# Kernel optimization log

Hardware: AMD Instinct MI355X
Metric: run time of the kernel (lower is better)

Reference implementation:

```python
import jax, jax.numpy as jnp
import numpy as np

# dims: L=seq_len, N=batch, C=embed_dim, H=heads, D=head_dim, W=window_size
L, N, C, H, D, W = 1024, 4, 2048, 16, 128, 512
ROPE_BASE = 10000.0
SCALE = 1.0 / np.sqrt(D).astype(np.float32)


def _rope(x, cos, sin):
    # interleaved-pair rotary embedding; x: (..., D), cos/sin broadcast to (..., D//2)
    x1, x2 = x[..., 0::2], x[..., 1::2]
    return jnp.stack([x1 * cos - x2 * sin, x1 * sin + x2 * cos], axis=-1).reshape(x.shape)


def setup_inputs() -> dict:
    key = jax.random.key(0)
    ks = jax.random.split(key, 4)
    s = 0.02
    return {
        "x": jax.random.normal(ks[0], (L, N, C), jnp.float32),
        "wq": jax.random.normal(ks[1], (C, C), jnp.float32) * s,
        "bq": jnp.zeros((C,), jnp.float32),
        "wkv": jax.random.normal(ks[2], (2 * C, C), jnp.float32) * s,
        "bkv": jnp.zeros((2 * C,), jnp.float32),
        "wo": jax.random.normal(ks[3], (C, C), jnp.float32) * s,
        "bo": jnp.zeros((C,), jnp.float32),
        "alibi_slopes": jnp.asarray(2.0 ** (-8.0 * np.arange(1, H + 1) / H), jnp.float32),
    }


def reference(x, wq, bq, wkv, bkv, wo, bo, alibi_slopes):
    # x: (L, N, C) -> batch-major (N, L, C)
    xb = jnp.transpose(x, (1, 0, 2))
    q = (xb @ wq.T + bq).reshape(N, L, H, D)
    # memory=None path: zero input cache, cache_mask all False
    cache = jnp.zeros((N, W, C), x.dtype)
    kv_cache = cache @ wkv.T + bkv          # detached in original; masked out anyway
    kv_cur = xb @ wkv.T + bkv
    kv = jnp.concatenate([kv_cache, kv_cur], axis=1).reshape(N, L + W, 2, H, D)
    # RoPE over absolute kv positions [0, L+W); queries live at positions [W, W+L)
    t = jnp.arange(L + W, dtype=jnp.float32)
    inv_freq = 1.0 / (ROPE_BASE ** (jnp.arange(0, D, 2, dtype=jnp.float32) / D))
    freqs = jnp.outer(t, inv_freq)          # (L+W, D//2)
    cos, sin = jnp.cos(freqs), jnp.sin(freqs)
    q = _rope(q, cos[W:W + L][None, :, None, :], sin[W:W + L][None, :, None, :])
    k = _rope(kv[:, :, 0], cos[None, :, None, :], sin[None, :, None, :])
    v = kv[:, :, 1]
    scores = jnp.einsum('bihd,bjhd->bhij', q, k) * SCALE  # (N,H,L,L+W)
    i = jnp.arange(L)[:, None]
    j = jnp.arange(L + W)[None, :]
    # causal sliding window: query at kv-position i+W attends j in [i, i+W];
    # kv_mask is False for the (empty) cache region j < W
    mask = (j >= i) & (j <= i + W) & (j >= W)
    bias = alibi_slopes[:, None, None] * (j - i - W).astype(jnp.float32)  # <= 0 in window
    scores = jnp.where(mask[None, None], scores + bias[None], -jnp.inf)
    p = jax.nn.softmax(scores, axis=-1)
    attn = jnp.einsum('bhij,bjhd->bihd', p, v).reshape(N, L, C)
    out = attn @ wo.T + bo
    return jnp.transpose(out, (1, 0, 2))    # (L, N, C)
```

## Files before the change

kernel.cpp:

```cpp
#include <hip/hip_runtime.h>
#include <hip/hip_bf16.h>

typedef __attribute__((ext_vector_type(4))) float f32x4;
typedef __attribute__((ext_vector_type(8))) short s16x8;
typedef __attribute__((ext_vector_type(4))) short s16x4;
typedef __attribute__((ext_vector_type(4))) int i32x4;

__device__ __forceinline__ short f2bf(float f) {
    union { __hip_bfloat16 h; short s; } u;
    u.h = __float2bfloat16(f);
    return u.s;
}

#define GLD16(g, l) __builtin_amdgcn_global_load_lds((const __attribute__((address_space(1))) void*)(g), (__attribute__((address_space(3))) void*)(l), 16, 0, 0)
#define MFMA16(a, b, c) __builtin_amdgcn_mfma_f32_16x16x32_bf16((a), (b), (c), 0, 0, 0)

__global__ void conv_lin(const float* __restrict__ in, short* __restrict__ out, int n4) {
    int i = blockIdx.x * blockDim.x + threadIdx.x;
    int stride = gridDim.x * blockDim.x;
    for (; i < n4; i += stride) {
        float4 v = reinterpret_cast<const float4*>(in)[i];
        s16x4 o;
        o[0] = f2bf(v.x); o[1] = f2bf(v.y); o[2] = f2bf(v.z); o[3] = f2bf(v.w);
        reinterpret_cast<s16x4*>(out)[i] = o;
    }
}

__global__ void conv_x(const float* __restrict__ x, short* __restrict__ Xb) {
    const int total = 1024 * 4 * 2048 / 4;
    int i = blockIdx.x * blockDim.x + threadIdx.x;
    int stride = gridDim.x * blockDim.x;
    for (; i < total; i += stride) {
        float4 v = reinterpret_cast<const float4*>(x)[i];
        int c4 = i & 511;
        int n  = (i >> 9) & 3;
        int l  = i >> 11;
        s16x4 o;
        o[0] = f2bf(v.x); o[1] = f2bf(v.y); o[2] = f2bf(v.z); o[3] = f2bf(v.w);
        reinterpret_cast<s16x4*>(Xb)[(n * 1024 + l) * 512 + c4] = o;
    }
}

__global__ void rope_tab(float* __restrict__ ctab, float* __restrict__ stab) {
    int l = blockIdx.x, t = threadIdx.x;
    float pos = (float)(512 + l);
    float inv = __expf(-9.210340371976184f * ((float)t * (1.0f / 64.0f)));
    float a = pos * inv;
    float s, c;
    sincosf(a, &s, &c);
    ctab[l * 64 + t] = c;
    stab[l * 64 + t] = s;
}

__device__ __forceinline__ void gemm128(const short* __restrict__ A, const short* __restrict__ B,
                                        short* As, short* Bs, f32x4 acc[4][4], int m0, int j0) {
    const int K = 2048;
    const int tid = threadIdx.x;
    const int lane = tid & 63;
    const int w = tid >> 6;
    const int wr = w >> 1, wc = w & 1;
    const int r8 = lane >> 3;
    const int cc = ((lane & 7) ^ r8) << 3;
    const size_t rowA0 = (size_t)(m0 + w * 32 + r8);
    const size_t rowB0 = (size_t)(j0 + w * 32 + r8);
    for (int kt = 0; kt < K; kt += 64) {
        #pragma unroll
        for (int q = 0; q < 4; ++q) {
            GLD16(A + (rowA0 + q * 8) * K + kt + cc, As + (w * 32 + q * 8) * 64);
            GLD16(B + (rowB0 + q * 8) * K + kt + cc, Bs + (w * 32 + q * 8) * 64);
        }
        __syncthreads();
        #pragma unroll
        for (int kk = 0; kk < 2; ++kk) {
            s16x8 af[4], bfv[4];
            #pragma unroll
            for (int mi = 0; mi < 4; ++mi) {
                int row = wr * 64 + mi * 16 + (lane & 15);
                int byte = row * 128 + ((kk * 64 + (lane >> 4) * 16) ^ ((row & 7) << 4));
                af[mi] = *reinterpret_cast<const s16x8*>(reinterpret_cast<const char*>(As) + byte);
            }
            #pragma unroll
            for (int nj = 0; nj < 4; ++nj) {
                int row = wc * 64 + nj * 16 + (lane & 15);
                int byte = row * 128 + ((kk * 64 + (lane >> 4) * 16) ^ ((row & 7) << 4));
                bfv[nj] = *reinterpret_cast<const s16x8*>(reinterpret_cast<const char*>(Bs) + byte);
            }
            #pragma unroll
            for (int mi = 0; mi < 4; ++mi)
                #pragma unroll
                for (int nj = 0; nj < 4; ++nj)
                    acc[mi][nj] = MFMA16(af[mi], bfv[nj], acc[mi][nj]);
        }
        __syncthreads();
    }
}

__global__ __launch_bounds__(256, 4)
void gemm_qkv(const short* __restrict__ Xb, const short* __restrict__ Wqkv,
              const float* __restrict__ bq, const float* __restrict__ bkv,
              const float* __restrict__ ctab, const float* __restrict__ stab,
              short* __restrict__ Qr, short* __restrict__ Kr, short* __restrict__ Vr) {
    __shared__ short As[8192], Bs[8192];
    const int m0 = blockIdx.y * 128, j0 = blockIdx.x * 128;
    f32x4 acc[4][4];
    #pragma unroll
    for (int a = 0; a < 4; ++a)
        #pragma unroll
        for (int b = 0; b < 4; ++b)
            #pragma unroll
            for (int r = 0; r < 4; ++r) acc[a][b][r] = 0.f;
    gemm128(Xb, Wqkv, As, Bs, acc, m0, j0);

    const int tid = threadIdx.x, lane = tid & 63, w = tid >> 6;
    const int wr = w >> 1, wc = w & 1;
    const int region = j0 >> 11;
    #pragma unroll
    for (int mi = 0; mi < 4; ++mi) {
        #pragma unroll
        for (int nj = 0; nj < 4; ++nj) {
            int col = j0 + wc * 64 + nj * 16 + (lane & 15);
            int h = (col >> 7) & 15;
            int d = col & 127;
            #pragma unroll
            for (int r = 0; r < 4; ++r) {
                int row = m0 + wr * 64 + mi * 16 + (lane >> 4) * 4 + r;
                int n = row >> 10, l = row & 1023;
                float v = acc[mi][nj][r];
                size_t oidx = (((size_t)(n * 16 + h)) * 1024 + l) * 128 + d;
                if (region == 0) {
                    v += bq[col];
                    float other = __shfl_xor(v, 1, 64);
                    float cs = ctab[l * 64 + (d >> 1)];
                    float sn = stab[l * 64 + (d >> 1)];
                    float o = (d & 1) ? (other * sn + v * cs) : (v * cs - other * sn);
                    Qr[oidx] = f2bf(o * 0.08838834764831843f);
                } else if (region == 1) {
                    v += bkv[col - 2048];
                    float other = __shfl_xor(v, 1, 64);
                    float cs = ctab[l * 64 + (d >> 1)];
                    float sn = stab[l * 64 + (d >> 1)];
                    float o = (d & 1) ? (other * sn + v * cs) : (v * cs - other * sn);
                    Kr[oidx] = f2bf(o);
                } else {
                    v += bkv[col - 2048];
                    Vr[oidx] = f2bf(v);
                }
            }
        }
    }
}

__global__ __launch_bounds__(256, 4)
void gemm_out(const short* __restrict__ Attn, const short* __restrict__ Wo,
              const float* __restrict__ bo, float* __restrict__ out) {
    __shared__ short As[8192], Bs[8192];
    const int m0 = blockIdx.y * 128, j0 = blockIdx.x * 128;
    f32x4 acc[4][4];
    #pragma unroll
    for (int a = 0; a < 4; ++a)
        #pragma unroll
        for (int b = 0; b < 4; ++b)
            #pragma unroll
            for (int r = 0; r < 4; ++r) acc[a][b][r] = 0.f;
    gemm128(Attn, Wo, As, Bs, acc, m0, j0);

    const int tid = threadIdx.x, lane = tid & 63, w = tid >> 6;
    const int wr = w >> 1, wc = w & 1;
    #pragma unroll
    for (int mi = 0; mi < 4; ++mi)
        #pragma unroll
        for (int nj = 0; nj < 4; ++nj) {
            int col = j0 + wc * 64 + nj * 16 + (lane & 15);
            #pragma unroll
            for (int r = 0; r < 4; ++r) {
                int row = m0 + wr * 64 + mi * 16 + (lane >> 4) * 4 + r;
                int n = row >> 10, l = row & 1023;
                out[((size_t)(l * 4 + n)) * 2048 + col] = acc[mi][nj][r] + bo[col];
            }
        }
}

__global__ __launch_bounds__(256, 2)
void attn_fwd(const short* __restrict__ Qr, const short* __restrict__ Kr,
              const short* __restrict__ Vr, const float* __restrict__ slopes,
              short* __restrict__ Attn) {
    __shared__ short Ks[64 * 128];
    __shared__ short Vts[128 * 64];
    __shared__ short Ps[4][2048];

    const int b = blockIdx.x;
    const int nh = (b & 7) * 8 + ((b >> 3) & 7);
    const int i0 = (b >> 6) * 128;
    const int n = nh >> 4, h = nh & 15;
    const short* Qh = Qr + (size_t)nh * (1024 * 128);
    const short* Kh = Kr + (size_t)nh * (1024 * 128);
    const short* Vh = Vr + (size_t)nh * (1024 * 128);
    const float slope = slopes[h];
    const int tid = threadIdx.x, lane = tid & 63, w = tid >> 6;

    s16x8 qf[2][4];
    #pragma unroll
    for (int mi = 0; mi < 2; ++mi)
        #pragma unroll
        for (int kk = 0; kk < 4; ++kk) {
            int row = i0 + w * 32 + mi * 16 + (lane & 15);
            qf[mi][kk] = *reinterpret_cast<const s16x8*>(Qh + (size_t)row * 128 + kk * 32 + (lane >> 4) * 8);
        }

    f32x4 oacc[2][8];
    #pragma unroll
    for (int mi = 0; mi < 2; ++mi)
        #pragma unroll
        for (int dj = 0; dj < 8; ++dj)
            #pragma unroll
            for (int r = 0; r < 4; ++r) oacc[mi][dj][r] = 0.f;
    float mrun[2][4], lrun[2][4];
    #pragma unroll
    for (int mi = 0; mi < 2; ++mi)
        #pragma unroll
        for (int r = 0; r < 4; ++r) { mrun[mi][r] = -1e30f; lrun[mi][r] = 0.f; }

    const int jlo = (i0 >= 512) ? (i0 - 512) : 0;
    const int jhi = i0 + 127;
    for (int j0 = jlo; j0 <= jhi; j0 += 64) {
        #pragma unroll
        for (int q = 0; q < 4; ++q) {
            int rbase = w * 16 + q * 4;
            int rloc = rbase + (lane >> 4);
            int lc = ((lane & 15) ^ (rloc & 7)) << 3;
            GLD16(Kh + (size_t)(j0 + rloc) * 128 + lc, Ks + rbase * 128);
        }
        #pragma unroll
        for (int p = 0; p < 4; ++p) {
            int d0 = (w + p * 4) * 8;
            int jj = j0 + lane;
            i32x4 vv = *reinterpret_cast<const i32x4*>(Vh + (size_t)jj * 128 + d0);
            const short* vs = reinterpret_cast<const short*>(&vv);
            #pragma unroll
            for (int e = 0; e < 8; ++e) {
                int d = d0 + e;
                int byte = d * 128 + ((lane * 2) ^ ((d & 7) << 4));
                *reinterpret_cast<short*>(reinterpret_cast<char*>(Vts) + byte) = vs[e];
            }
        }
        __syncthreads();

        f32x4 sacc[2][4];
        #pragma unroll
        for (int mi = 0; mi < 2; ++mi)
            #pragma unroll
            for (int nj = 0; nj < 4; ++nj)
                #pragma unroll
                for (int r = 0; r < 4; ++r) sacc[mi][nj][r] = 0.f;
        #pragma unroll
        for (int kk = 0; kk < 4; ++kk) {
            s16x8 kf[4];
            #pragma unroll
            for (int nj = 0; nj < 4; ++nj) {
                int kr = nj * 16 + (lane & 15);
                int byte = kr * 256 + ((kk * 64 + (lane >> 4) * 16) ^ ((kr & 7) << 4));
                kf[nj] = *reinterpret_cast<const s16x8*>(reinterpret_cast<const char*>(Ks) + byte);
            }
            #pragma unroll
            for (int mi = 0; mi < 2; ++mi)
                #pragma unroll
                for (int nj = 0; nj < 4; ++nj)
                    sacc[mi][nj] = MFMA16(qf[mi][kk], kf[nj], sacc[mi][nj]);
        }

        #pragma unroll
        for (int mi = 0; mi < 2; ++mi) {
            #pragma unroll
            for (int r = 0; r < 4; ++r) {
                int iq = i0 + w * 32 + mi * 16 + (lane >> 4) * 4 + r;
                float mx = -1e30f;
                #pragma unroll
                for (int nj = 0; nj < 4; ++nj) {
                    int jj = j0 + nj * 16 + (lane & 15);
                    float v = -1e30f;
                    if (jj <= iq && jj >= iq - 512)
                        v = sacc[mi][nj][r] + slope * (float)(jj - iq);
                    sacc[mi][nj][r] = v;
                    mx = fmaxf(mx, v);
                }
                #pragma unroll
                for (int s = 1; s < 16; s <<= 1) mx = fmaxf(mx, __shfl_xor(mx, s, 64));
                float mnew = fmaxf(mrun[mi][r], mx);
                float sf = __expf(mrun[mi][r] - mnew);
                mrun[mi][r] = mnew;
                lrun[mi][r] *= sf;
                #pragma unroll
                for (int dj = 0; dj < 8; ++dj) oacc[mi][dj][r] *= sf;
                float rs = 0.f;
                #pragma unroll
                for (int nj = 0; nj < 4; ++nj) {
                    float v = sacc[mi][nj][r];
                    float p = (v < -1e29f) ? 0.f : __expf(v - mnew);
                    sacc[mi][nj][r] = p;
                    rs += p;
                }
                #pragma unroll
                for (int s = 1; s < 16; s <<= 1) rs += __shfl_xor(rs, s, 64);
                lrun[mi][r] += rs;
            }
        }

        char* Pw = reinterpret_cast<char*>(&Ps[w][0]);
        #pragma unroll
        for (int mi = 0; mi < 2; ++mi)
            #pragma unroll
            for (int nj = 0; nj < 4; ++nj)
                #pragma unroll
                for (int r = 0; r < 4; ++r) {
                    int prow = mi * 16 + (lane >> 4) * 4 + r;
                    int cb = (nj * 16 + (lane & 15)) * 2;
                    int byte = prow * 128 + (cb ^ ((prow & 7) << 4));
                    *reinterpret_cast<short*>(Pw + byte) = f2bf(sacc[mi][nj][r]);
                }

        #pragma unroll
        for (int ks = 0; ks < 2; ++ks) {
            s16x8 pf[2];
            #pragma unroll
            for (int mi = 0; mi < 2; ++mi) {
                int prow = mi * 16 + (lane & 15);
                int byte = prow * 128 + (((ks * 32 + (lane >> 4) * 8) * 2) ^ ((prow & 7) << 4));
                pf[mi] = *reinterpret_cast<const s16x8*>(Pw + byte);
            }
            #pragma unroll
            for (int dj = 0; dj < 8; ++dj) {
                int d = dj * 16 + (lane & 15);
                int byte = d * 128 + (((ks * 32 + (lane >> 4) * 8) * 2) ^ ((d & 7) << 4));
                s16x8 vf = *reinterpret_cast<const s16x8*>(reinterpret_cast<const char*>(Vts) + byte);
                #pragma unroll
                for (int mi = 0; mi < 2; ++mi)
                    oacc[mi][dj] = MFMA16(pf[mi], vf, oacc[mi][dj]);
            }
        }
        __syncthreads();
    }

    #pragma unroll
    for (int mi = 0; mi < 2; ++mi)
        #pragma unroll
        for (int dj = 0; dj < 8; ++dj)
            #pragma unroll
            for (int r = 0; r < 4; ++r) {
                int iq = i0 + w * 32 + mi * 16 + (lane >> 4) * 4 + r;
                int d = dj * 16 + (lane & 15);
                float v = oacc[mi][dj][r] / lrun[mi][r];
                Attn[((size_t)(n * 1024 + iq)) * 2048 + h * 128 + d] = f2bf(v);
            }
}

extern "C" void kernel_launch(void* const* d_in, const int* in_sizes, int n_in,
                              void* d_out, int out_size, void* d_ws, size_t ws_size,
                              hipStream_t stream) {
    const float* x      = (const float*)d_in[0];
    const float* wq     = (const float*)d_in[1];
    const float* bq     = (const float*)d_in[2];
    const float* wkv    = (const float*)d_in[3];
    const float* bkv    = (const float*)d_in[4];
    const float* wo     = (const float*)d_in[5];
    const float* bo     = (const float*)d_in[6];
    const float* slopes = (const float*)d_in[7];
    float* out = (float*)d_out;

    char* ws = (char*)d_ws;
    size_t off = 0;
    auto alloc = [&](size_t bytes) { char* p = ws + off; off += (bytes + 255) & ~(size_t)255; return p; };
    float* ctab = (float*)alloc((size_t)1024 * 64 * 4);
    float* stab = (float*)alloc((size_t)1024 * 64 * 4);
    short* Xb   = (short*)alloc((size_t)4096 * 2048 * 2);
    short* Wqkv = (short*)alloc((size_t)6144 * 2048 * 2);
    short* Wo   = (short*)alloc((size_t)2048 * 2048 * 2);
    short* Qr   = (short*)alloc((size_t)64 * 1024 * 128 * 2);
    short* Kr   = (short*)alloc((size_t)64 * 1024 * 128 * 2);
    short* Vr   = (short*)alloc((size_t)64 * 1024 * 128 * 2);
    short* Attn = (short*)alloc((size_t)4096 * 2048 * 2);

    conv_x<<<2048, 256, 0, stream>>>(x, Xb);
    conv_lin<<<1024, 256, 0, stream>>>(wq, Wqkv, 2048 * 2048 / 4);
    conv_lin<<<2048, 256, 0, stream>>>(wkv, Wqkv + (size_t)2048 * 2048, 4096 * 2048 / 4);
    conv_lin<<<1024, 256, 0, stream>>>(wo, Wo, 2048 * 2048 / 4);
    rope_tab<<<1024, 64, 0, stream>>>(ctab, stab);
    gemm_qkv<<<dim3(48, 32), 256, 0, stream>>>(Xb, Wqkv, bq, bkv, ctab, stab, Qr, Kr, Vr);
    attn_fwd<<<512, 256, 0, stream>>>(Qr, Kr, Vr, slopes, Attn);
    gemm_out<<<dim3(16, 32), 256, 0, stream>>>(Attn, Wo, bo, out);
}
```

Baseline: 244.8 us.

## Pipeline QKV and output GEMMs with 8-wave 256x128 tiles and multi-stage LDS

Replaces the single-buffered 128x128 GEMM core with an 8-wave (512-thread) 256x128 tile that double-buffers K slices in LDS. Global-to-LDS loads for future slices are issued while MFMAs run, with manual waitcnt, barriers and setprio. Blocks are remapped to a 1D grid with an XCD-aware swizzle across column tiles. This aims to hide memory latency and improve L2 locality, but the epilogue still indexes only 4 waves' worth of rows (wr = w>>1 now spans 0..3 with 64-row stride, matching a 256-row tile), so correctness depends on that mapping holding.

```diff
diff --git a/kernel.cpp b/kernel.cpp
--- a/kernel.cpp
+++ b/kernel.cpp
@@ -52,64 +52,92 @@
     stab[l * 64 + t] = s;
 }
 
-__device__ __forceinline__ void gemm128(const short* __restrict__ A, const short* __restrict__ B,
-                                        short* As, short* Bs, f32x4 acc[4][4], int m0, int j0) {
-    const int K = 2048;
-    const int tid = threadIdx.x;
-    const int lane = tid & 63;
-    const int w = tid >> 6;
-    const int wr = w >> 1, wc = w & 1;
-    const int r8 = lane >> 3;
-    const int cc = ((lane & 7) ^ r8) << 3;
-    const size_t rowA0 = (size_t)(m0 + w * 32 + r8);
-    const size_t rowB0 = (size_t)(j0 + w * 32 + r8);
-    for (int kt = 0; kt < K; kt += 64) {
-        #pragma unroll
-        for (int q = 0; q < 4; ++q) {
-            GLD16(A + (rowA0 + q * 8) * K + kt + cc, As + (w * 32 + q * 8) * 64);
-            GLD16(B + (rowB0 + q * 8) * K + kt + cc, Bs + (w * 32 + q * 8) * 64);
-        }
-        __syncthreads();
-        #pragma unroll
-        for (int kk = 0; kk < 2; ++kk) {
-            s16x8 af[4], bfv[4];
-            #pragma unroll
-            for (int mi = 0; mi < 4; ++mi) {
-                int row = wr * 64 + mi * 16 + (lane & 15);
-                int byte = row * 128 + ((kk * 64 + (lane >> 4) * 16) ^ ((row & 7) << 4));
-                af[mi] = *reinterpret_cast<const s16x8*>(reinterpret_cast<const char*>(As) + byte);
-            }
-            #pragma unroll
-            for (int nj = 0; nj < 4; ++nj) {
-                int row = wc * 64 + nj * 16 + (lane & 15);
-                int byte = row * 128 + ((kk * 64 + (lane >> 4) * 16) ^ ((row & 7) << 4));
-                bfv[nj] = *reinterpret_cast<const s16x8*>(reinterpret_cast<const char*>(Bs) + byte);
-            }
-            #pragma unroll
-            for (int mi = 0; mi < 4; ++mi)
-                #pragma unroll
-                for (int nj = 0; nj < 4; ++nj)
-                    acc[mi][nj] = MFMA16(af[mi], bfv[nj], acc[mi][nj]);
-        }
-        __syncthreads();
-    }
-}
-
-__global__ __launch_bounds__(256, 4)
+
+__device__ __forceinline__ void stageA(const short* __restrict__ G, int rowbase, int kbase,
+                                       short* dst, int tid) {
+    #pragma unroll
+    for (int q = 0; q < 2; ++q) {
+        int chunk = q * 512 + tid;
+        GLD16(G + (size_t)(rowbase + (chunk >> 2)) * 2048 + kbase + ((chunk & 3) << 3),
+              dst + q * 4096 + (tid & ~63) * 8);
+    }
+}
+__device__ __forceinline__ void stageB(const short* __restrict__ G, int rowbase, int kbase,
+                                       short* dst, int tid) {
+    GLD16(G + (size_t)(rowbase + (tid >> 2)) * 2048 + kbase + ((tid & 3) << 3),
+          dst + (tid & ~63) * 8);
+}
+
+__device__ __forceinline__ void gemm_core8(const short* __restrict__ Aop, const short* __restrict__ Bop,
+                                           short* AL, short* BL, f32x4 acc[4][4], int m0, int j0) {
+    const int tid = threadIdx.x, lane = tid & 63;
+    const int w = tid >> 6, wr = w >> 1, wc = w & 1;
+
+    auto STG = [&](int sk, int skh) {
+        int kb = (sk & 31) * 64 + skh * 32;
+        stageA(Aop, m0, kb, AL + (sk & 1) * 16384 + skh * 8192, tid);
+        stageB(Bop, j0, kb, BL + (sk & 1) * 8192 + skh * 4096, tid);
+    };
+
+    auto PHASE = [&](int kk, int ks, int sk, int skh) {
+        const short* Ar = AL + (kk & 1) * 16384 + ks * 8192;
+        const short* Br = BL + (kk & 1) * 8192 + ks * 4096;
+        s16x8 af[4], bfv[4];
+        #pragma unroll
+        for (int mi = 0; mi < 4; ++mi)
+            af[mi] = *reinterpret_cast<const s16x8*>(Ar + (wr * 64 + mi * 16 + (lane & 15)) * 32 + (lane >> 4) * 8);
+        #pragma unroll
+        for (int nj = 0; nj < 4; ++nj)
+            bfv[nj] = *reinterpret_cast<const s16x8*>(Br + (wc * 64 + nj * 16 + (lane & 15)) * 32 + (lane >> 4) * 8);
+        STG(sk, skh);
+        asm volatile("s_waitcnt vmcnt(6)" ::: "memory");
+        __builtin_amdgcn_s_barrier();
+        asm volatile("s_waitcnt lgkmcnt(0)" ::: "memory");
+        __builtin_amdgcn_sched_barrier(0);
+        __builtin_amdgcn_s_setprio(1);
+        #pragma unroll
+        for (int mi = 0; mi < 4; ++mi)
+            #pragma unroll
+            for (int nj = 0; nj < 4; ++nj)
+                acc[mi][nj] = MFMA16(af[mi], bfv[nj], acc[mi][nj]);
+        __builtin_amdgcn_s_setprio(0);
+        __builtin_amdgcn_s_barrier();
+    };
+
+    STG(0, 0); STG(0, 1); STG(1, 0);
+    asm volatile("s_waitcnt vmcnt(3)" ::: "memory");
+    __builtin_amdgcn_s_barrier();
+
+    for (int t = 0; t < 16; ++t) {
+        const int k0 = 2 * t, k1 = 2 * t + 1;
+        PHASE(k0, 0, k1, 1);
+        PHASE(k0, 1, k0 + 2, 0);
+        PHASE(k1, 0, k0 + 2, 1);
+        PHASE(k1, 1, k0 + 3, 0);
+    }
+    asm volatile("s_waitcnt vmcnt(0)" ::: "memory");
+}
+
+__global__ __launch_bounds__(512, 2)
 void gemm_qkv(const short* __restrict__ Xb, const short* __restrict__ Wqkv,
               const float* __restrict__ bq, const float* __restrict__ bkv,
               const float* __restrict__ ctab, const float* __restrict__ stab,
               short* __restrict__ Qr, short* __restrict__ Kr, short* __restrict__ Vr) {
-    __shared__ short As[8192], Bs[8192];
-    const int m0 = blockIdx.y * 128, j0 = blockIdx.x * 128;
+    __shared__ short AL[2 * 2 * 8192];
+    __shared__ short BL[2 * 2 * 4096];
+    const int b = blockIdx.x;
+    const int i = b >> 3;
+    const int m0 = (i / 6) * 256;
+    const int j0 = ((i % 6) + (b & 7) * 6) * 128;
+
     f32x4 acc[4][4];
     #pragma unroll
     for (int a = 0; a < 4; ++a)
         #pragma unroll
-        for (int b = 0; b < 4; ++b)
-            #pragma unroll
-            for (int r = 0; r < 4; ++r) acc[a][b][r] = 0.f;
-    gemm128(Xb, Wqkv, As, Bs, acc, m0, j0);
+        for (int c = 0; c < 4; ++c)
+            #pragma unroll
+            for (int r = 0; r < 4; ++r) acc[a][c][r] = 0.f;
+    gemm_core8(Xb, Wqkv, AL, BL, acc, m0, j0);
 
     const int tid = threadIdx.x, lane = tid & 63, w = tid >> 6;
     const int wr = w >> 1, wc = w & 1;
@@ -150,19 +178,24 @@
     }
 }
 
-__global__ __launch_bounds__(256, 4)
+__global__ __launch_bounds__(512, 2)
 void gemm_out(const short* __restrict__ Attn, const short* __restrict__ Wo,
               const float* __restrict__ bo, float* __restrict__ out) {
-    __shared__ short As[8192], Bs[8192];
-    const int m0 = blockIdx.y * 128, j0 = blockIdx.x * 128;
+    __shared__ short AL[2 * 2 * 8192];
+    __shared__ short BL[2 * 2 * 4096];
+    const int b = blockIdx.x;
+    const int i = b >> 3;
+    const int m0 = (i / 2) * 256;
+    const int j0 = ((i % 2) + (b & 7) * 2) * 128;
+
     f32x4 acc[4][4];
     #pragma unroll
     for (int a = 0; a < 4; ++a)
         #pragma unroll
-        for (int b = 0; b < 4; ++b)
-            #pragma unroll
-            for (int r = 0; r < 4; ++r) acc[a][b][r] = 0.f;
-    gemm128(Attn, Wo, As, Bs, acc, m0, j0);
+        for (int c = 0; c < 4; ++c)
+            #pragma unroll
+            for (int r = 0; r < 4; ++r) acc[a][c][r] = 0.f;
+    gemm_core8(Attn, Wo, AL, BL, acc, m0, j0);
 
     const int tid = threadIdx.x, lane = tid & 63, w = tid >> 6;
     const int wr = w >> 1, wc = w & 1;
@@ -384,7 +417,7 @@
     conv_lin<<<2048, 256, 0, stream>>>(wkv, Wqkv + (size_t)2048 * 2048, 4096 * 2048 / 4);
     conv_lin<<<1024, 256, 0, stream>>>(wo, Wo, 2048 * 2048 / 4);
     rope_tab<<<1024, 64, 0, stream>>>(ctab, stab);
-    gemm_qkv<<<dim3(48, 32), 256, 0, stream>>>(Xb, Wqkv, bq, bkv, ctab, stab, Qr, Kr, Vr);
+    gemm_qkv<<<768, 512, 0, stream>>>(Xb, Wqkv, bq, bkv, ctab, stab, Qr, Kr, Vr);
     attn_fwd<<<512, 256, 0, stream>>>(Qr, Kr, Vr, slopes, Attn);
-    gemm_out<<<dim3(16, 32), 256, 0, stream>>>(Attn, Wo, bo, out);
-}
+    gemm_out<<<256, 512, 0, stream>>>(Attn, Wo, bo, out);
+}
```

After: 297.9 us. +21.7%, slower.

## Pair adjacent lanes for wider epilogue stores and merge weight conversions

Applied to the files above, without the earlier changes.

The epilogues of the QKV GEMM, attention and output GEMM now swap values between adjacent lanes, and even lanes write 32-bit (bf16 pairs) or 64-bit (float pairs) stores, replacing 16-bit and 32-bit scalar stores. The aim is fewer store instructions and better write coalescing. The three weight-conversion launches are also merged into one kernel to cut launch overhead. The cost is an extra cross-lane shuffle per element and half the lanes sitting idle during the store.

```diff
diff --git a/kernel.cpp b/kernel.cpp
--- a/kernel.cpp
+++ b/kernel.cpp
@@ -15,14 +15,31 @@
 #define GLD16(g, l) __builtin_amdgcn_global_load_lds((const __attribute__((address_space(1))) void*)(g), (__attribute__((address_space(3))) void*)(l), 16, 0, 0)
 #define MFMA16(a, b, c) __builtin_amdgcn_mfma_f32_16x16x32_bf16((a), (b), (c), 0, 0, 0)
 
-__global__ void conv_lin(const float* __restrict__ in, short* __restrict__ out, int n4) {
+__global__ void conv_w(const float* __restrict__ wq, const float* __restrict__ wkv,
+                       const float* __restrict__ wo, short* __restrict__ Wqkv,
+                       short* __restrict__ Wo) {
+    const int n1 = 2048 * 2048 / 4;
+    const int n2 = 4096 * 2048 / 4;
+    const int n3 = 2048 * 2048 / 4;
+    const int total = n1 + n2 + n3;
     int i = blockIdx.x * blockDim.x + threadIdx.x;
     int stride = gridDim.x * blockDim.x;
-    for (; i < n4; i += stride) {
-        float4 v = reinterpret_cast<const float4*>(in)[i];
+    for (; i < total; i += stride) {
+        float4 v;
+        s16x4* dst;
+        if (i < n1) {
+            v = reinterpret_cast<const float4*>(wq)[i];
+            dst = reinterpret_cast<s16x4*>(Wqkv) + i;
+        } else if (i < n1 + n2) {
+            v = reinterpret_cast<const float4*>(wkv)[i - n1];
+            dst = reinterpret_cast<s16x4*>(Wqkv) + i;
+        } else {
+            v = reinterpret_cast<const float4*>(wo)[i - n1 - n2];
+            dst = reinterpret_cast<s16x4*>(Wo) + (i - n1 - n2);
+        }
         s16x4 o;
         o[0] = f2bf(v.x); o[1] = f2bf(v.y); o[2] = f2bf(v.z); o[3] = f2bf(v.w);
-        reinterpret_cast<s16x4*>(out)[i] = o;
+        *dst = o;
     }
 }
 
@@ -114,6 +131,7 @@
     const int tid = threadIdx.x, lane = tid & 63, w = tid >> 6;
     const int wr = w >> 1, wc = w & 1;
     const int region = j0 >> 11;
+    const bool evenlane = !(lane & 1);
     #pragma unroll
     for (int mi = 0; mi < 4; ++mi) {
         #pragma unroll
@@ -133,17 +151,29 @@
                     float cs = ctab[l * 64 + (d >> 1)];
                     float sn = stab[l * 64 + (d >> 1)];
                     float o = (d & 1) ? (other * sn + v * cs) : (v * cs - other * sn);
-                    Qr[oidx] = f2bf(o * 0.08838834764831843f);
+                    int sown = (unsigned short)f2bf(o * 0.08838834764831843f);
+                    int spart = __shfl_xor(sown, 1, 64);
+                    if (evenlane)
+                        *reinterpret_cast<unsigned int*>(Qr + oidx) =
+                            (unsigned int)sown | ((unsigned int)spart << 16);
                 } else if (region == 1) {
                     v += bkv[col - 2048];
                     float other = __shfl_xor(v, 1, 64);
                     float cs = ctab[l * 64 + (d >> 1)];
                     float sn = stab[l * 64 + (d >> 1)];
                     float o = (d & 1) ? (other * sn + v * cs) : (v * cs - other * sn);
-                    Kr[oidx] = f2bf(o);
+                    int sown = (unsigned short)f2bf(o);
+                    int spart = __shfl_xor(sown, 1, 64);
+                    if (evenlane)
+                        *reinterpret_cast<unsigned int*>(Kr + oidx) =
+                            (unsigned int)sown | ((unsigned int)spart << 16);
                 } else {
                     v += bkv[col - 2048];
-                    Vr[oidx] = f2bf(v);
+                    int sown = (unsigned short)f2bf(v);
+                    int spart = __shfl_xor(sown, 1, 64);
+                    if (evenlane)
+                        *reinterpret_cast<unsigned int*>(Vr + oidx) =
+                            (unsigned int)sown | ((unsigned int)spart << 16);
                 }
             }
         }
@@ -166,6 +196,7 @@
 
     const int tid = threadIdx.x, lane = tid & 63, w = tid >> 6;
     const int wr = w >> 1, wc = w & 1;
+    const bool evenlane = !(lane & 1);
     #pragma unroll
     for (int mi = 0; mi < 4; ++mi)
         #pragma unroll
@@ -175,7 +206,12 @@
             for (int r = 0; r < 4; ++r) {
                 int row = m0 + wr * 64 + mi * 16 + (lane >> 4) * 4 + r;
                 int n = row >> 10, l = row & 1023;
-                out[((size_t)(l * 4 + n)) * 2048 + col] = acc[mi][nj][r] + bo[col];
+                float fown = acc[mi][nj][r] + bo[col];
+                float fpart = __shfl_xor(fown, 1, 64);
+                if (evenlane) {
+                    float2 p = make_float2(fown, fpart);
+                    *reinterpret_cast<float2*>(&out[((size_t)(l * 4 + n)) * 2048 + col]) = p;
+                }
             }
         }
 }
@@ -340,6 +376,7 @@
         __syncthreads();
     }
 
+    const bool evenlane = !(lane & 1);
     #pragma unroll
     for (int mi = 0; mi < 2; ++mi)
         #pragma unroll
@@ -349,7 +386,12 @@
                 int iq = i0 + w * 32 + mi * 16 + (lane >> 4) * 4 + r;
                 int d = dj * 16 + (lane & 15);
                 float v = oacc[mi][dj][r] / lrun[mi][r];
-                Attn[((size_t)(n * 1024 + iq)) * 2048 + h * 128 + d] = f2bf(v);
+                int sown = (unsigned short)f2bf(v);
+                int spart = __shfl_xor(sown, 1, 64);
+                if (evenlane)
+                    *reinterpret_cast<unsigned int*>(
+                        &Attn[((size_t)(n * 1024 + iq)) * 2048 + h * 128 + d]) =
+                        (unsigned int)sown | ((unsigned int)spart << 16);
             }
 }
 
@@ -380,9 +422,7 @@
     short* Attn = (short*)alloc((size_t)4096 * 2048 * 2);
 
     conv_x<<<2048, 256, 0, stream>>>(x, Xb);
-    conv_lin<<<1024, 256, 0, stream>>>(wq, Wqkv, 2048 * 2048 / 4);
-    conv_lin<<<2048, 256, 0, stream>>>(wkv, Wqkv + (size_t)2048 * 2048, 4096 * 2048 / 4);
-    conv_lin<<<1024, 256, 0, stream>>>(wo, Wo, 2048 * 2048 / 4);
+    conv_w<<<2048, 256, 0, stream>>>(wq, wkv, wo, Wqkv, Wo);
     rope_tab<<<1024, 64, 0, stream>>>(ctab, stab);
     gemm_qkv<<<dim3(48, 32), 256, 0, stream>>>(Xb, Wqkv, bq, bkv, ctab, stab, Qr, Kr, Vr);
     attn_fwd<<<512, 256, 0, stream>>>(Qr, Kr, Vr, slopes, Attn);
```

New measurement: 257.8 us. +5.3%, slower.

## Rewrite QKV GEMM as 256x256 tile, 8-wave kernel with double-buffered prefetch

Applied to the files above, without the earlier changes.

Replaces the 128x128, 4-wave QKV projection GEMM with a 256x256 tile kernel using 512 threads and double-buffered LDS. It issues global-to-LDS loads for the next K-slab interleaved with MFMA phases, using explicit vmcnt waits, barriers and setprio. The goal is to hide load latency behind compute and raise arithmetic intensity per tile. The cost is more LDS (128KB per block), heavier register use for 8x4 accumulators, and fewer blocks (384) across the GPU, which may hurt occupancy and tail balance.

```diff
diff --git a/kernel.cpp b/kernel.cpp
--- a/kernel.cpp
+++ b/kernel.cpp
@@ -52,70 +52,110 @@
     stab[l * 64 + t] = s;
 }
 
-__device__ __forceinline__ void gemm128(const short* __restrict__ A, const short* __restrict__ B,
-                                        short* As, short* Bs, f32x4 acc[4][4], int m0, int j0) {
-    const int K = 2048;
-    const int tid = threadIdx.x;
-    const int lane = tid & 63;
-    const int w = tid >> 6;
-    const int wr = w >> 1, wc = w & 1;
-    const int r8 = lane >> 3;
-    const int cc = ((lane & 7) ^ r8) << 3;
-    const size_t rowA0 = (size_t)(m0 + w * 32 + r8);
-    const size_t rowB0 = (size_t)(j0 + w * 32 + r8);
-    for (int kt = 0; kt < K; kt += 64) {
-        #pragma unroll
-        for (int q = 0; q < 4; ++q) {
-            GLD16(A + (rowA0 + q * 8) * K + kt + cc, As + (w * 32 + q * 8) * 64);
-            GLD16(B + (rowB0 + q * 8) * K + kt + cc, Bs + (w * 32 + q * 8) * 64);
-        }
-        __syncthreads();
-        #pragma unroll
-        for (int kk = 0; kk < 2; ++kk) {
-            s16x8 af[4], bfv[4];
-            #pragma unroll
-            for (int mi = 0; mi < 4; ++mi) {
-                int row = wr * 64 + mi * 16 + (lane & 15);
-                int byte = row * 128 + ((kk * 64 + (lane >> 4) * 16) ^ ((row & 7) << 4));
-                af[mi] = *reinterpret_cast<const s16x8*>(reinterpret_cast<const char*>(As) + byte);
-            }
-            #pragma unroll
-            for (int nj = 0; nj < 4; ++nj) {
-                int row = wc * 64 + nj * 16 + (lane & 15);
-                int byte = row * 128 + ((kk * 64 + (lane >> 4) * 16) ^ ((row & 7) << 4));
-                bfv[nj] = *reinterpret_cast<const s16x8*>(reinterpret_cast<const char*>(Bs) + byte);
-            }
-            #pragma unroll
-            for (int mi = 0; mi < 4; ++mi)
-                #pragma unroll
-                for (int nj = 0; nj < 4; ++nj)
-                    acc[mi][nj] = MFMA16(af[mi], bfv[nj], acc[mi][nj]);
-        }
-        __syncthreads();
-    }
-}
-
-__global__ __launch_bounds__(256, 4)
-void gemm_qkv(const short* __restrict__ Xb, const short* __restrict__ Wqkv,
-              const float* __restrict__ bq, const float* __restrict__ bkv,
-              const float* __restrict__ ctab, const float* __restrict__ stab,
-              short* __restrict__ Qr, short* __restrict__ Kr, short* __restrict__ Vr) {
-    __shared__ short As[8192], Bs[8192];
-    const int m0 = blockIdx.y * 128, j0 = blockIdx.x * 128;
-    f32x4 acc[4][4];
-    #pragma unroll
-    for (int a = 0; a < 4; ++a)
-        #pragma unroll
-        for (int b = 0; b < 4; ++b)
-            #pragma unroll
-            for (int r = 0; r < 4; ++r) acc[a][b][r] = 0.f;
-    gemm128(Xb, Wqkv, As, Bs, acc, m0, j0);
-
+
+__device__ __forceinline__ void stg_half(const short* __restrict__ G, int rowbase, int kt,
+                                         short* dst, int tid) {
+    #pragma unroll
+    for (int q = 0; q < 2; ++q) {
+        int chunk = q * 512 + tid;
+        int row = chunk >> 3;
+        int sc = ((((chunk & 7) << 4) ^ ((row & 7) << 4)) >> 1);
+        GLD16(G + (size_t)(rowbase + row) * 2048 + kt + sc, dst + (q * 512 + (tid & ~63)) * 8);
+    }
+}
+
+__device__ __forceinline__ s16x8 rdf(const short* buf, int row, int ks, int lane) {
+    int byte = row * 128 + (((ks << 6) + ((lane >> 4) << 4)) ^ ((row & 7) << 4));
+    return *reinterpret_cast<const s16x8*>(reinterpret_cast<const char*>(buf) + byte);
+}
+
+#define PH(D, Q, VMN, ...)                                                            \
+    {                                                                                  \
+        const short* Ah = &Al[D][wr][0];                                               \
+        const short* Bh = &Bl[D][wc >> 1][0];                                          \
+        if (Q == 0) {                                                                  \
+            _Pragma("unroll")                                                          \
+            for (int nj = 0; nj < 4; ++nj) {                                           \
+                bf[nj][0] = rdf(Bh, (wc & 1) * 64 + nj * 16 + (lane & 15), 0, lane);   \
+                bf[nj][1] = rdf(Bh, (wc & 1) * 64 + nj * 16 + (lane & 15), 1, lane);   \
+            }                                                                          \
+        }                                                                              \
+        s16x8 af[2][2];                                                                \
+        _Pragma("unroll")                                                              \
+        for (int m = 0; m < 2; ++m) {                                                  \
+            af[m][0] = rdf(Ah, (Q * 2 + m) * 16 + (lane & 15), 0, lane);               \
+            af[m][1] = rdf(Ah, (Q * 2 + m) * 16 + (lane & 15), 1, lane);               \
+        }                                                                              \
+        __VA_ARGS__;                                                                   \
+        if ((VMN) == 4) { asm volatile("s_waitcnt vmcnt(4)" ::: "memory");             \
+                          __builtin_amdgcn_sched_barrier(0); }                         \
+        if ((VMN) == 0) { asm volatile("s_waitcnt vmcnt(0)" ::: "memory");             \
+                          __builtin_amdgcn_sched_barrier(0); }                         \
+        __builtin_amdgcn_s_barrier();                                                  \
+        asm volatile("s_waitcnt lgkmcnt(0)" ::: "memory");                             \
+        __builtin_amdgcn_sched_barrier(0);                                             \
+        __builtin_amdgcn_s_setprio(1);                                                 \
+        _Pragma("unroll")                                                              \
+        for (int m = 0; m < 2; ++m)                                                    \
+            _Pragma("unroll")                                                          \
+            for (int nj = 0; nj < 4; ++nj) {                                           \
+                acc[Q * 2 + m][nj] = MFMA16(af[m][0], bf[nj][0], acc[Q * 2 + m][nj]);  \
+                acc[Q * 2 + m][nj] = MFMA16(af[m][1], bf[nj][1], acc[Q * 2 + m][nj]);  \
+            }                                                                          \
+        __builtin_amdgcn_s_setprio(0);                                                 \
+        __builtin_amdgcn_s_barrier();                                                  \
+        __builtin_amdgcn_sched_barrier(0);                                             \
+    }
+
+__global__ __launch_bounds__(512, 2)
+void gemm_qkv8(const short* __restrict__ Xb, const short* __restrict__ Wqkv,
+               const float* __restrict__ bq, const float* __restrict__ bkv,
+               const float* __restrict__ ctab, const float* __restrict__ stab,
+               short* __restrict__ Qr, short* __restrict__ Kr, short* __restrict__ Vr) {
+    __shared__ short Al[2][2][8192];
+    __shared__ short Bl[2][2][8192];
     const int tid = threadIdx.x, lane = tid & 63, w = tid >> 6;
-    const int wr = w >> 1, wc = w & 1;
+    const int wr = w >> 2, wc = w & 3;
+    const int m0 = blockIdx.y * 256, j0 = blockIdx.x * 256;
+
+    f32x4 acc[8][4];
+    #pragma unroll
+    for (int a = 0; a < 8; ++a)
+        #pragma unroll
+        for (int c = 0; c < 4; ++c)
+            #pragma unroll
+            for (int r = 0; r < 4; ++r) acc[a][c][r] = 0.f;
+
+    stg_half(Xb,   m0,        0, &Al[0][0][0], tid);
+    stg_half(Xb,   m0 + 128,  0, &Al[0][1][0], tid);
+    stg_half(Wqkv, j0,        0, &Bl[0][0][0], tid);
+    stg_half(Wqkv, j0 + 128,  0, &Bl[0][1][0], tid);
+    stg_half(Wqkv, j0,       64, &Bl[1][0][0], tid);
+    stg_half(Wqkv, j0 + 128, 64, &Bl[1][1][0], tid);
+    asm volatile("s_waitcnt vmcnt(4)" ::: "memory");
+    __builtin_amdgcn_s_barrier();
+    __builtin_amdgcn_sched_barrier(0);
+
+    s16x8 bf[4][2];
+    for (int u = 0; u < 16; ++u) {
+        const int ka = (2 * u + 1) * 64;
+        const int kb = (2 * u + 2) * 64;
+        const int kc = (2 * u + 3) * 64;
+        const bool s = (u < 15);
+        PH(0, 0, -1, stg_half(Xb, m0,       ka, &Al[1][0][0], tid));
+        PH(0, 1, -1, stg_half(Xb, m0 + 128, ka, &Al[1][1][0], tid));
+        PH(0, 2, -1, if (s) stg_half(Wqkv, j0,       kb, &Bl[0][0][0], tid));
+        PH(0, 3, (s ? 4 : 0), if (s) stg_half(Wqkv, j0 + 128, kb, &Bl[0][1][0], tid));
+        PH(1, 0, -1, if (s) stg_half(Xb, m0,       kb, &Al[0][0][0], tid));
+        PH(1, 1, -1, if (s) stg_half(Xb, m0 + 128, kb, &Al[0][1][0], tid));
+        PH(1, 2, -1, if (s) stg_half(Wqkv, j0,       kc, &Bl[1][0][0], tid));
+        PH(1, 3, (s ? 4 : 0), if (s) stg_half(Wqkv, j0 + 128, kc, &Bl[1][1][0], tid));
+    }
+    asm volatile("s_waitcnt vmcnt(0)" ::: "memory");
+
     const int region = j0 >> 11;
     #pragma unroll
-    for (int mi = 0; mi < 4; ++mi) {
+    for (int mi = 0; mi < 8; ++mi) {
         #pragma unroll
         for (int nj = 0; nj < 4; ++nj) {
             int col = j0 + wc * 64 + nj * 16 + (lane & 15);
@@ -123,7 +163,7 @@
             int d = col & 127;
             #pragma unroll
             for (int r = 0; r < 4; ++r) {
-                int row = m0 + wr * 64 + mi * 16 + (lane >> 4) * 4 + r;
+                int row = m0 + wr * 128 + mi * 16 + (lane >> 4) * 4 + r;
                 int n = row >> 10, l = row & 1023;
                 float v = acc[mi][nj][r];
                 size_t oidx = (((size_t)(n * 16 + h)) * 1024 + l) * 128 + d;
@@ -150,6 +190,49 @@
     }
 }
 
+__device__ __forceinline__ void gemm128(const short* __restrict__ A, const short* __restrict__ B,
+                                        short* As, short* Bs, f32x4 acc[4][4], int m0, int j0) {
+    const int K = 2048;
+    const int tid = threadIdx.x;
+    const int lane = tid & 63;
+    const int w = tid >> 6;
+    const int wr = w >> 1, wc = w & 1;
+    const int r8 = lane >> 3;
+    const int cc = ((lane & 7) ^ r8) << 3;
+    const size_t rowA0 = (size_t)(m0 + w * 32 + r8);
+    const size_t rowB0 = (size_t)(j0 + w * 32 + r8);
+    for (int kt = 0; kt < K; kt += 64) {
+        #pragma unroll
+        for (int q = 0; q < 4; ++q) {
+            GLD16(A + (rowA0 + q * 8) * K + kt + cc, As + (w * 32 + q * 8) * 64);
+            GLD16(B + (rowB0 + q * 8) * K + kt + cc, Bs + (w * 32 + q * 8) * 64);
+        }
+        __syncthreads();
+        #pragma unroll
+        for (int kk = 0; kk < 2; ++kk) {
+            s16x8 af[4], bfv[4];
+            #pragma unroll
+            for (int mi = 0; mi < 4; ++mi) {
+                int row = wr * 64 + mi * 16 + (lane & 15);
+                int byte = row * 128 + ((kk * 64 + (lane >> 4) * 16) ^ ((row & 7) << 4));
+                af[mi] = *reinterpret_cast<const s16x8*>(reinterpret_cast<const char*>(As) + byte);
+            }
+            #pragma unroll
+            for (int nj = 0; nj < 4; ++nj) {
+                int row = wc * 64 + nj * 16 + (lane & 15);
+                int byte = row * 128 + ((kk * 64 + (lane >> 4) * 16) ^ ((row & 7) << 4));
+                bfv[nj] = *reinterpret_cast<const s16x8*>(reinterpret_cast<const char*>(Bs) + byte);
+            }
+            #pragma unroll
+            for (int mi = 0; mi < 4; ++mi)
+                #pragma unroll
+                for (int nj = 0; nj < 4; ++nj)
+                    acc[mi][nj] = MFMA16(af[mi], bfv[nj], acc[mi][nj]);
+        }
+        __syncthreads();
+    }
+}
+
 __global__ __launch_bounds__(256, 4)
 void gemm_out(const short* __restrict__ Attn, const short* __restrict__ Wo,
               const float* __restrict__ bo, float* __restrict__ out) {
@@ -384,7 +467,7 @@
     conv_lin<<<2048, 256, 0, stream>>>(wkv, Wqkv + (size_t)2048 * 2048, 4096 * 2048 / 4);
     conv_lin<<<1024, 256, 0, stream>>>(wo, Wo, 2048 * 2048 / 4);
     rope_tab<<<1024, 64, 0, stream>>>(ctab, stab);
-    gemm_qkv<<<dim3(48, 32), 256, 0, stream>>>(Xb, Wqkv, bq, bkv, ctab, stab, Qr, Kr, Vr);
+    gemm_qkv8<<<dim3(24, 16), 512, 0, stream>>>(Xb, Wqkv, bq, bkv, ctab, stab, Qr, Kr, Vr);
     attn_fwd<<<512, 256, 0, stream>>>(Qr, Kr, Vr, slopes, Attn);
     gemm_out<<<dim3(16, 32), 256, 0, stream>>>(Attn, Wo, bo, out);
 }
```

After: 290.7 us. +18.7%, slower.
